# Optimization experiments

Hardware: AMD Instinct MI355X
Metric: run time of the kernel (lower is better)

## Reference

```python
import jax, jax.numpy as jnp
import numpy as np

B, NQ = 4, 4096
HF, WF = 96, 96          # single-level feature map -> Nv = 9216
NV = HF * WF
E = 768                  # dim * num_frames = 192 * 4
NH, NP, NL = 8, 4, 1
HD = E // NH             # 96
EPS = 1e-6


def _layer_norm(x, w, b):
    m = jnp.mean(x, axis=-1, keepdims=True)
    v = jnp.var(x, axis=-1, keepdims=True)
    return (x - m) * jax.lax.rsqrt(v + EPS) * w + b


def _msda_core(value, shapes, loc, aw):
    # value: (B, Nv, H, D); loc: (B, Nq, H, L, P, 2) normalized in [0,1];
    # aw: (B, Nq, H, L, P). Bilinear sampling matching F.grid_sample
    # (align_corners=False, padding_mode='zeros'): pixel = loc * size - 0.5.
    Bn, Nv, H, D = value.shape
    Nq, P = loc.shape[1], loc.shape[4]
    out = jnp.zeros((Bn, H, Nq, D), value.dtype)
    start = 0
    for lvl in range(shapes.shape[0]):
        Hl, Wl = int(shapes[lvl, 0]), int(shapes[lvl, 1])
        v = value[:, start:start + Hl * Wl].transpose(0, 2, 1, 3)  # (B,H,S,D)
        start += Hl * Wl
        x = loc[:, :, :, lvl, :, 0] * Wl - 0.5  # (B,Nq,H,P)
        y = loc[:, :, :, lvl, :, 1] * Hl - 0.5
        x0, y0 = jnp.floor(x), jnp.floor(y)
        sampled = jnp.zeros((Bn, H, Nq, P, D), value.dtype)
        for dx in (0, 1):
            for dy in (0, 1):
                xi, yi = x0 + dx, y0 + dy
                w = (1.0 - jnp.abs(x - xi)) * (1.0 - jnp.abs(y - yi))
                valid = (xi >= 0) & (xi <= Wl - 1) & (yi >= 0) & (yi <= Hl - 1)
                idx = (jnp.clip(yi, 0, Hl - 1) * Wl
                       + jnp.clip(xi, 0, Wl - 1)).astype(jnp.int32)
                idx = idx.transpose(0, 2, 1, 3).reshape(Bn, H, Nq * P)
                g = jnp.take_along_axis(v, idx[..., None], axis=2)
                g = g.reshape(Bn, H, Nq, P, D)
                wz = jnp.where(valid, w, 0.0).transpose(0, 2, 1, 3)[..., None]
                sampled = sampled + g * wz
        awl = aw[:, :, :, lvl].transpose(0, 2, 1, 3)[..., None]  # (B,H,Nq,P,1)
        out = out + jnp.sum(sampled * awl, axis=3)
    return out.transpose(0, 2, 1, 3).reshape(Bn, Nq, H * D)


def setup_inputs():
    key = jax.random.key(0)
    ks = jax.random.split(key, 12)
    s = 0.02
    return {
        "query": jax.random.normal(ks[0], (B, NQ, E), jnp.float32),
        "reference_points": jax.random.uniform(ks[1], (B, NQ, NL, 2), jnp.float32),
        "feat": jax.random.normal(ks[2], (B, NV, E), jnp.float32),
        "spatial_shapes": jnp.array([[HF, WF]], jnp.int32),
        "level_start_index": jnp.zeros((NL,), jnp.int32),
        "ln_q_w": jnp.ones((E,), jnp.float32),
        "ln_q_b": jnp.zeros((E,), jnp.float32),
        "ln_f_w": jnp.ones((E,), jnp.float32),
        "ln_f_b": jnp.zeros((E,), jnp.float32),
        "W_value": jax.random.normal(ks[3], (E, E), jnp.float32) * s,
        "b_value": jnp.zeros((E,), jnp.float32),
        "W_off": jax.random.normal(ks[4], (E, NH * NL * NP * 2), jnp.float32) * s,
        "b_off": jax.random.normal(ks[5], (NH * NL * NP * 2,), jnp.float32) * s,
        "W_attn": jax.random.normal(ks[6], (E, NH * NL * NP), jnp.float32) * s,
        "b_attn": jnp.zeros((NH * NL * NP,), jnp.float32),
        "W_out": jax.random.normal(ks[7], (E, E), jnp.float32) * s,
        "b_out": jnp.zeros((E,), jnp.float32),
        "gamma": jax.random.normal(ks[8], (E,), jnp.float32) * s,
    }


def reference(query, reference_points, feat, spatial_shapes, level_start_index,
              ln_q_w, ln_q_b, ln_f_w, ln_f_b, W_value, b_value, W_off, b_off,
              W_attn, b_attn, W_out, b_out, gamma):
    shapes = np.asarray(spatial_shapes)  # static level shapes
    Bn, Nq, _ = query.shape
    Nv = feat.shape[1]
    q = _layer_norm(query, ln_q_w, ln_q_b)
    f = _layer_norm(feat, ln_f_w, ln_f_b)
    value = (f @ W_value + b_value).reshape(Bn, Nv, NH, HD)
    offsets = (q @ W_off + b_off).reshape(Bn, Nq, NH, NL, NP, 2)
    aw = jax.nn.softmax((q @ W_attn + b_attn).reshape(Bn, Nq, NH, NL * NP), -1)
    aw = aw.reshape(Bn, Nq, NH, NL, NP)
    # offset_normalizer = [W_l, H_l] per level
    norm = jnp.stack([jnp.asarray(shapes[:, 1], jnp.float32),
                      jnp.asarray(shapes[:, 0], jnp.float32)], axis=-1)  # (L,2)
    loc = (reference_points[:, :, None, :, None, :]
           + offsets / norm[None, None, None, :, None, :])
    out = _msda_core(value, shapes, loc, aw)
    out = out @ W_out + b_out
    attn = q + out  # mmcv MSDeformAttn adds identity (dropout=eval no-op)
    return query + gamma * attn
```

## Files before the change

kernel.cpp:

```cpp
#include <hip/hip_runtime.h>

#define BB     4
#define NQS    4096
#define NVS    9216
#define E_DIM  768
#define NHEAD  8
#define NPTS   4
#define HDIM   96
#define HFEAT  96
#define WFEAT  96
#define MQR    16384
#define NLNB   13312
#define NTRB   1152
#define NVALB  432

typedef __attribute__((ext_vector_type(8))) short  s8v;
typedef __attribute__((ext_vector_type(4))) short  s4v;
typedef __attribute__((ext_vector_type(4))) float  f4v;

__device__ __forceinline__ unsigned short f2bf(float x) {
    unsigned int u = __builtin_bit_cast(unsigned int, x);
    unsigned int r = (u + 0x7fffu + ((u >> 16) & 1u)) >> 16;
    return (unsigned short)r;
}
__device__ __forceinline__ float bf2f(unsigned short s) {
    unsigned int u = ((unsigned int)s) << 16;
    return __builtin_bit_cast(float, u);
}
__device__ __forceinline__ float bf2f_s(short s) {
    return bf2f((unsigned short)s);
}

#define GLD16(gp, lp) \
    __builtin_amdgcn_global_load_lds( \
        (__attribute__((address_space(1))) void*)(gp), \
        (__attribute__((address_space(3))) void*)(lp), 16, 0, 0)

__global__ __launch_bounds__(256) void prep_kernel(
    const float* __restrict__ q, const float* __restrict__ f,
    const float* __restrict__ qw, const float* __restrict__ qb,
    const float* __restrict__ fw, const float* __restrict__ fb,
    unsigned short* __restrict__ qout, unsigned short* __restrict__ fout,
    float* __restrict__ stats,
    const float* __restrict__ W0, const float* __restrict__ W1,
    unsigned short* __restrict__ T0, unsigned short* __restrict__ T1,
    const float* __restrict__ W_off, const float* __restrict__ W_attn,
    const float* __restrict__ b_off, const float* __restrict__ b_attn,
    unsigned short* __restrict__ Wqc, float* __restrict__ bcat) {
    __shared__ float tile[32][33];
    const int bid = blockIdx.x;

    if (bid < NLNB) {
        const int wv = threadIdx.x >> 6, lane = threadIdx.x & 63;
        const int row = bid * 4 + wv;
        const bool isq = row < MQR;
        const float* x = isq ? (q + (size_t)row * E_DIM)
                             : (f + (size_t)(row - MQR) * E_DIM);
        const float4 v0 = ((const float4*)x)[lane];
        const float4 v1 = ((const float4*)x)[lane + 64];
        const float4 v2 = ((const float4*)x)[lane + 128];
        float s1 = v0.x + v0.y + v0.z + v0.w + v1.x + v1.y + v1.z + v1.w
                 + v2.x + v2.y + v2.z + v2.w;
        float s2 = v0.x * v0.x + v0.y * v0.y + v0.z * v0.z + v0.w * v0.w
                 + v1.x * v1.x + v1.y * v1.y + v1.z * v1.z + v1.w * v1.w
                 + v2.x * v2.x + v2.y * v2.y + v2.z * v2.z + v2.w * v2.w;
        #pragma unroll
        for (int o = 32; o > 0; o >>= 1) {
            s1 += __shfl_down(s1, o, 64);
            s2 += __shfl_down(s2, o, 64);
        }
        const float mean = __shfl(s1, 0, 64) * (1.0f / E_DIM);
        const float m2   = __shfl(s2, 0, 64) * (1.0f / E_DIM);
        const float rstd = rsqrtf(m2 - mean * mean + 1e-6f);
        if (isq && lane == 0) { stats[row * 2] = mean; stats[row * 2 + 1] = rstd; }
        const float* w = isq ? qw : fw;
        const float* b = isq ? qb : fb;
        unsigned short* o = isq ? (qout + (size_t)row * E_DIM)
                                : (fout + (size_t)(row - MQR) * E_DIM);
        const float4 vv[3] = {v0, v1, v2};
        #pragma unroll
        for (int c = 0; c < 3; c++) {
            const float4 w4 = ((const float4*)w)[lane + c * 64];
            const float4 b4 = ((const float4*)b)[lane + c * 64];
            s4v ov;
            ov[0] = (short)f2bf((vv[c].x - mean) * rstd * w4.x + b4.x);
            ov[1] = (short)f2bf((vv[c].y - mean) * rstd * w4.y + b4.y);
            ov[2] = (short)f2bf((vv[c].z - mean) * rstd * w4.z + b4.z);
            ov[3] = (short)f2bf((vv[c].w - mean) * rstd * w4.w + b4.w);
            ((s4v*)o)[lane + c * 64] = ov;
        }
    } else if (bid < NLNB + NTRB) {
        const int idx = bid - NLNB;
        const int z = idx / 576, r2 = idx - z * 576;
        const float* W = z ? W1 : W0;
        unsigned short* Wt = z ? T1 : T0;
        const int bi = (r2 / 24) * 32, bj = (r2 % 24) * 32;
        const int t = threadIdx.x;
        const int r = t >> 5, c = t & 31;
        #pragma unroll
        for (int i = 0; i < 4; i++)
            tile[r + i * 8][c] = W[(size_t)(bi + r + i * 8) * E_DIM + bj + c];
        __syncthreads();
        #pragma unroll
        for (int i = 0; i < 4; i++)
            Wt[(size_t)(bj + r + i * 8) * E_DIM + bi + c] = f2bf(tile[c][r + i * 8]);
    } else {
        const int idx = (bid - NLNB - NTRB) * 256 + threadIdx.x;
        const int rrow = idx / E_DIM, k = idx % E_DIM;
        float v = 0.f;
        if (rrow < 64) v = W_off[(size_t)k * 64 + rrow];
        else if (rrow < 96) v = W_attn[(size_t)k * 32 + (rrow - 64)];
        Wqc[idx] = f2bf(v);
        if (idx < 128) {
            float b = 0.f;
            if (idx < 64) b = b_off[idx];
            else if (idx < 96) b = b_attn[idx - 64];
            bcat[idx] = b;
        }
    }
}

__global__ __launch_bounds__(256, 3) void mfma_gemm128(
    const unsigned short* __restrict__ A, const unsigned short* __restrict__ Bt,
    const float* __restrict__ bias, float* __restrict__ C, int ldC,
    const float* __restrict__ query, const float* __restrict__ qstats,
    const float* __restrict__ lnw, const float* __restrict__ lnb,
    const float* __restrict__ gamma) {
    __shared__ unsigned short As[128 * 64];
    __shared__ unsigned short Bs[128 * 64];

    constexpr int K = E_DIM;
    const int tid = threadIdx.x;
    const int wave = tid >> 6;
    const int lane = tid & 63;
    const int quad = lane >> 4;
    const int l16 = lane & 15;

    const int nwg = gridDim.x * gridDim.y;
    const int flat = blockIdx.y * gridDim.x + blockIdx.x;
    const int cpx = nwg >> 3;
    const int swz = (flat & 7) * cpx + (flat >> 3);
    const int bx = swz % gridDim.x;
    const int by = swz / gridDim.x;
    const int bm = by * 128;
    const int bn = bx * 128;
    const int wrow = wave >> 1, wcol = wave & 1;

    const unsigned short* arow[4];
    const unsigned short* brow[4];
    unsigned short* aldst[4];
    unsigned short* bldst[4];
    #pragma unroll
    for (int i = 0; i < 4; i++) {
        const int chunk = wave * 4 + i;
        const int s = chunk >> 1, r = (chunk & 1) * 64 + lane;
        arow[i] = A + (size_t)(bm + r) * K + s * 8;
        brow[i] = Bt + (size_t)(bn + r) * K + s * 8;
        aldst[i] = As + chunk * 512;
        bldst[i] = Bs + chunk * 512;
    }

    f4v acc[4][4] = {};

    for (int k0 = 0; k0 < K; k0 += 64) {
        #pragma unroll
        for (int i = 0; i < 4; i++)
            GLD16(arow[i] + k0, aldst[i]);
        #pragma unroll
        for (int i = 0; i < 4; i++)
            GLD16(brow[i] + k0, bldst[i]);

        __syncthreads();

        #pragma unroll
        for (int c = 0; c < 2; c++) {
            s8v af[4], bf[4];
            #pragma unroll
            for (int ti = 0; ti < 4; ti++)
                af[ti] = *(const s8v*)(As + ((size_t)((c * 4 + quad) * 128 + wrow * 64 + ti * 16 + l16)) * 8);
            #pragma unroll
            for (int tj = 0; tj < 4; tj++)
                bf[tj] = *(const s8v*)(Bs + ((size_t)((c * 4 + quad) * 128 + wcol * 64 + tj * 16 + l16)) * 8);
            #pragma unroll
            for (int ti = 0; ti < 4; ti++)
                #pragma unroll
                for (int tj = 0; tj < 4; tj++)
                    acc[ti][tj] = __builtin_amdgcn_mfma_f32_16x16x32_bf16(af[ti], bf[tj], acc[ti][tj], 0, 0, 0);
        }
        __syncthreads();
    }

    #pragma unroll
    for (int ti = 0; ti < 4; ti++) {
        const int gm_base = bm + wrow * 64 + ti * 16 + quad * 4;
        #pragma unroll
        for (int tj = 0; tj < 4; tj++) {
            const int gn = bn + wcol * 64 + tj * 16 + l16;
            const float bv = bias[gn];
            #pragma unroll
            for (int r = 0; r < 4; r++) {
                const int gm = gm_base + r;
                const float v = acc[ti][tj][r] + bv;
                const size_t idx = (size_t)gm * ldC + gn;
                const float qv = query[idx];
                const float qln = (qv - qstats[gm * 2]) * qstats[gm * 2 + 1] * lnw[gn] + lnb[gn];
                C[idx] = qv + gamma[gn] * (qln + v);
            }
        }
    }
}

template <int G>
__device__ __forceinline__ void tigroup(const unsigned short* as_, const s8v (&bfr)[2][4],
                                        f4v (&acc)[8][4], int quad, int l16, int wrow) {
    s8v af[2][2];
    #pragma unroll
    for (int c = 0; c < 2; c++)
        #pragma unroll
        for (int m = 0; m < 2; m++)
            af[c][m] = *(const s8v*)(as_ + ((size_t)((c * 4 + quad) * 256 + wrow * 128 + (G * 2 + m) * 16 + l16)) * 8);
    #pragma unroll
    for (int c = 0; c < 2; c++)
        #pragma unroll
        for (int m = 0; m < 2; m++)
            #pragma unroll
            for (int n = 0; n < 4; n++)
                acc[G * 2 + m][n] = __builtin_amdgcn_mfma_f32_16x16x32_bf16(
                    af[c][m], bfr[c][n], acc[G * 2 + m][n], 0, 0, 0);
}

__global__ __launch_bounds__(512, 2) void mfma_gemm256(
    const unsigned short* __restrict__ A, const unsigned short* __restrict__ Bt,
    const float* __restrict__ bias, unsigned short* __restrict__ C,
    const unsigned short* __restrict__ Aq, const unsigned short* __restrict__ Wqc,
    const float* __restrict__ bcat, float* __restrict__ offattn) {
    __shared__ unsigned short As[2][256 * 64];
    __shared__ unsigned short Bs[2][256 * 64];

    constexpr int K = E_DIM;
    constexpr int NT = K / 64;
    const int tid = threadIdx.x;
    const int wave = tid >> 6;
    const int lane = tid & 63;
    const int quad = lane >> 4;
    const int l16 = lane & 15;

    if (blockIdx.x < NVALB) {
        const int flat = blockIdx.x;
        const int cpx = NVALB >> 3;
        const int swz = (flat & 7) * cpx + (flat >> 3);
        const int bx = swz % 3;
        const int by = swz / 3;
        const int bm = by * 256;
        const int bn = bx * 256;
        const int wrow = wave >> 2;
        const int wcol = wave & 3;

        const unsigned short* gsrc[4][2];
        int ldst[4][2];
        #pragma unroll
        for (int h = 0; h < 4; h++) {
            #pragma unroll
            for (int i = 0; i < 2; i++) {
                const int ch = wave * 2 + i;
                const int s = ch >> 1, rsub = ch & 1;
                const int rw = (h & 1) * 128 + rsub * 64 + lane;
                const unsigned short* base = (h < 2) ? (A + (size_t)(bm + rw) * K)
                                                     : (Bt + (size_t)(bn + rw) * K);
                gsrc[h][i] = base + s * 8;
                ldst[h][i] = (s * 256 + rw) * 8;
            }
        }

        #define STAGE256(h, kt, buf) do { \
            unsigned short* lb_ = ((h) < 2 ? &As[(buf)][0] : &Bs[(buf)][0]); \
            GLD16(gsrc[h][0] + (size_t)(kt) * 64, lb_ + ldst[h][0]); \
            GLD16(gsrc[h][1] + (size_t)(kt) * 64, lb_ + ldst[h][1]); \
        } while (0)

        f4v acc[8][4] = {};

        #pragma unroll
        for (int h = 0; h < 4; h++) STAGE256(h, 0, 0);

        int cur = 0;
        for (int t = 0; t < NT; ++t) {
            const unsigned short* as_ = &As[cur][0];
            const unsigned short* bs_ = &Bs[cur][0];
            const int nb = cur ^ 1;
            const bool pf = (t + 1 < NT);

            if (pf) {
                STAGE256(0, t + 1, nb);
                asm volatile("s_waitcnt vmcnt(2)" ::: "memory");
            } else {
                asm volatile("s_waitcnt vmcnt(0)" ::: "memory");
            }
            __builtin_amdgcn_s_barrier();
            __builtin_amdgcn_sched_barrier(0);

            s8v bfr[2][4];
            #pragma unroll
            for (int c = 0; c < 2; c++)
                #pragma unroll
                for (int n = 0; n < 4; n++)
                    bfr[c][n] = *(const s8v*)(bs_ + ((size_t)((c * 4 + quad) * 256 + wcol * 64 + n * 16 + l16)) * 8);

            __builtin_amdgcn_s_setprio(1);
            tigroup<0>(as_, bfr, acc, quad, l16, wrow);
            __builtin_amdgcn_s_setprio(0);

            if (pf) STAGE256(1, t + 1, nb);
            __builtin_amdgcn_s_setprio(1);
            tigroup<1>(as_, bfr, acc, quad, l16, wrow);
            __builtin_amdgcn_s_setprio(0);

            if (pf) STAGE256(2, t + 1, nb);
            __builtin_amdgcn_s_setprio(1);
            tigroup<2>(as_, bfr, acc, quad, l16, wrow);
            __builtin_amdgcn_s_setprio(0);

            if (pf) STAGE256(3, t + 1, nb);
            s8v af3[2][2];
            #pragma unroll
            for (int c = 0; c < 2; c++)
                #pragma unroll
                for (int m = 0; m < 2; m++)
                    af3[c][m] = *(const s8v*)(as_ + ((size_t)((c * 4 + quad) * 256 + wrow * 128 + (6 + m) * 16 + l16)) * 8);
            asm volatile("s_waitcnt lgkmcnt(0)" ::: "memory");
            __builtin_amdgcn_sched_barrier(0);
            __builtin_amdgcn_s_barrier();
            __builtin_amdgcn_sched_barrier(0);
            __builtin_amdgcn_s_setprio(1);
            #pragma unroll
            for (int c = 0; c < 2; c++)
                #pragma unroll
                for (int m = 0; m < 2; m++)
                    #pragma unroll
                    for (int n = 0; n < 4; n++)
                        acc[6 + m][n] = __builtin_amdgcn_mfma_f32_16x16x32_bf16(
                            af3[c][m], bfr[c][n], acc[6 + m][n], 0, 0, 0);
            __builtin_amdgcn_s_setprio(0);

            cur ^= 1;
        }
        #undef STAGE256

        #pragma unroll
        for (int ti = 0; ti < 8; ti++) {
            const int gm_base = bm + wrow * 128 + ti * 16 + quad * 4;
            #pragma unroll
            for (int tj = 0; tj < 4; tj++) {
                const int gn = bn + wcol * 64 + tj * 16 + l16;
                const float bv = bias[gn];
                const int hh = gn / HDIM, dd = gn - hh * HDIM;
                #pragma unroll
                for (int r = 0; r < 4; r++) {
                    const int gm = gm_base + r;
                    const float v = acc[ti][tj][r] + bv;
                    const int b = gm / NVS, s = gm - b * NVS;
                    const size_t vidx = (((size_t)b * NHEAD + hh) * NVS + s) * HDIM + dd;
                    C[vidx] = f2bf(v);
                }
            }
        }
    } else {
        const int bm = (blockIdx.x - NVALB) * 128;
        const int wrow = wave >> 2;
        const int wcol = wave & 3;
        unsigned short* As0 = &As[0][0];
        unsigned short* Bs0 = &Bs[0][0];

        const unsigned short* arow[2];
        const unsigned short* brow[2];
        int loff[2];
        #pragma unroll
        for (int i = 0; i < 2; i++) {
            const int ch = wave * 2 + i;
            const int s = ch >> 1, r = (ch & 1) * 64 + lane;
            arow[i] = Aq + (size_t)(bm + r) * K + s * 8;
            brow[i] = Wqc + (size_t)r * K + s * 8;
            loff[i] = (s * 128 + r) * 8;
        }

        f4v accq[4][2] = {};

        for (int k0 = 0; k0 < K; k0 += 64) {
            #pragma unroll
            for (int i = 0; i < 2; i++) GLD16(arow[i] + k0, As0 + loff[i]);
            #pragma unroll
            for (int i = 0; i < 2; i++) GLD16(brow[i] + k0, Bs0 + loff[i]);

            __syncthreads();

            #pragma unroll
            for (int c = 0; c < 2; c++) {
                s8v af[4], bf[2];
                #pragma unroll
                for (int m = 0; m < 4; m++)
                    af[m] = *(const s8v*)(As0 + ((size_t)((c * 4 + quad) * 128 + wrow * 64 + m * 16 + l16)) * 8);
                #pragma unroll
                for (int n = 0; n < 2; n++)
                    bf[n] = *(const s8v*)(Bs0 + ((size_t)((c * 4 + quad) * 128 + wcol * 32 + n * 16 + l16)) * 8);
                #pragma unroll
                for (int m = 0; m < 4; m++)
                    #pragma unroll
                    for (int n = 0; n < 2; n++)
                        accq[m][n] = __builtin_amdgcn_mfma_f32_16x16x32_bf16(af[m], bf[n], accq[m][n], 0, 0, 0);
            }
            __syncthreads();
        }

        #pragma unroll
        for (int m = 0; m < 4; m++) {
            const int gm_base = bm + wrow * 64 + m * 16 + quad * 4;
            #pragma unroll
            for (int n = 0; n < 2; n++) {
                const int gn = wcol * 32 + n * 16 + l16;
                const float bv = bcat[gn];
                #pragma unroll
                for (int r = 0; r < 4; r++)
                    offattn[(size_t)(gm_base + r) * 128 + gn] = accq[m][n][r] + bv;
            }
        }
    }
}

__global__ __launch_bounds__(384) void msda_kernel(
    const unsigned short* __restrict__ value,
    const float* __restrict__ oa,
    const float* __restrict__ refp,
    unsigned short* __restrict__ out) {
    const int h = blockIdx.x;
    const int row0 = blockIdx.y * 32;
    const int t = threadIdx.x;

    __shared__ float x_s[128], y_s[128], aw_s[128];
    if (t < 128) {
        const int r = t >> 2, p = t & 3;
        const int row = row0 + r;
        const float* oar = oa + (size_t)row * 128;
        float a = oar[64 + h * 4 + p];
        float mx = fmaxf(a, __shfl_xor(a, 1, 64));
        mx = fmaxf(mx, __shfl_xor(mx, 2, 64));
        float e = __expf(a - mx);
        float sden = e + __shfl_xor(e, 1, 64);
        sden += __shfl_xor(sden, 2, 64);
        aw_s[t] = e / sden;
        const float rx = refp[(size_t)row * 2 + 0] * WFEAT - 0.5f;
        const float ry = refp[(size_t)row * 2 + 1] * HFEAT - 0.5f;
        x_s[t] = rx + oar[h * 8 + p * 2 + 0];
        y_s[t] = ry + oar[h * 8 + p * 2 + 1];
    }
    __syncthreads();

    const int r = t / 12;
    const int j = t - r * 12;
    const int row = row0 + r;
    const int b = row >> 12;
    const unsigned short* vb = value + ((size_t)(b * NHEAD + h) * NVS) * HDIM + j * 8;

    float acc[8] = {};
    #pragma unroll
    for (int p = 0; p < 4; p++) {
        const float x = x_s[r * 4 + p];
        const float y = y_s[r * 4 + p];
        const float aw = aw_s[r * 4 + p];
        const float x0f = floorf(x), y0f = floorf(y);
        const float fx = x - x0f, fy = y - y0f;
        const int ix0 = (int)x0f, iy0 = (int)y0f;
        const int ix1 = ix0 + 1, iy1 = iy0 + 1;
        const float wx0 = (ix0 >= 0 && ix0 < WFEAT) ? (1.f - fx) : 0.f;
        const float wx1 = (ix1 >= 0 && ix1 < WFEAT) ? fx : 0.f;
        const float wy0 = (iy0 >= 0 && iy0 < HFEAT) ? (1.f - fy) : 0.f;
        const float wy1 = (iy1 >= 0 && iy1 < HFEAT) ? fy : 0.f;
        const int cx0 = min(max(ix0, 0), WFEAT - 1);
        const int cx1 = min(max(ix1, 0), WFEAT - 1);
        const int cy0 = min(max(iy0, 0), HFEAT - 1);
        const int cy1 = min(max(iy1, 0), HFEAT - 1);
        const float w00 = aw * wy0 * wx0, w01 = aw * wy0 * wx1;
        const float w10 = aw * wy1 * wx0, w11 = aw * wy1 * wx1;
        const s8v v00 = *(const s8v*)(vb + (size_t)(cy0 * WFEAT + cx0) * HDIM);
        const s8v v01 = *(const s8v*)(vb + (size_t)(cy0 * WFEAT + cx1) * HDIM);
        const s8v v10 = *(const s8v*)(vb + (size_t)(cy1 * WFEAT + cx0) * HDIM);
        const s8v v11 = *(const s8v*)(vb + (size_t)(cy1 * WFEAT + cx1) * HDIM);
        #pragma unroll
        for (int k = 0; k < 8; k++) {
            acc[k] += w00 * bf2f_s(v00[k]) + w01 * bf2f_s(v01[k])
                    + w10 * bf2f_s(v10[k]) + w11 * bf2f_s(v11[k]);
        }
    }

    s8v o;
    #pragma unroll
    for (int k = 0; k < 8; k++) o[k] = (short)f2bf(acc[k]);
    *(s8v*)(out + (size_t)row * E_DIM + h * HDIM + j * 8) = o;
}

extern "C" void kernel_launch(void* const* d_in, const int* in_sizes, int n_in,
                              void* d_out, int out_size, void* d_ws, size_t ws_size,
                              hipStream_t stream) {
    (void)in_sizes; (void)n_in; (void)out_size; (void)ws_size;

    const float* query  = (const float*)d_in[0];
    const float* refp   = (const float*)d_in[1];
    const float* feat   = (const float*)d_in[2];
    const float* ln_q_w = (const float*)d_in[5];
    const float* ln_q_b = (const float*)d_in[6];
    const float* ln_f_w = (const float*)d_in[7];
    const float* ln_f_b = (const float*)d_in[8];
    const float* W_val  = (const float*)d_in[9];
    const float* b_val  = (const float*)d_in[10];
    const float* W_off  = (const float*)d_in[11];
    const float* b_off  = (const float*)d_in[12];
    const float* W_attn = (const float*)d_in[13];
    const float* b_attn = (const float*)d_in[14];
    const float* W_out  = (const float*)d_in[15];
    const float* b_out  = (const float*)d_in[16];
    const float* gamma  = (const float*)d_in[17];
    float* out = (float*)d_out;

    const int MQ = BB * NQS;
    const int MV = BB * NVS;

    char* ws = (char*)d_ws;
    float*          q_stats = (float*)(ws + 0);
    unsigned short* qbf     = (unsigned short*)(ws + 131072);
    unsigned short* fbf     = (unsigned short*)(ws + 25296896);
    unsigned short* val_bf  = (unsigned short*)(ws + 81920000);
    unsigned short* msda_bf = (unsigned short*)(ws + 138543104);
    float*          offattn = (float*)(ws + 163708928);
    unsigned short* Wv_t    = (unsigned short*)(ws + 172097536);
    unsigned short* Wo_t    = (unsigned short*)(ws + 173277184);
    unsigned short* Wqc_t   = (unsigned short*)(ws + 174456832);
    float*          bcat    = (float*)(ws + 174653440);

    prep_kernel<<<NLNB + NTRB + 384, 256, 0, stream>>>(
        query, feat, ln_q_w, ln_q_b, ln_f_w, ln_f_b, qbf, fbf, q_stats,
        W_val, W_out, Wv_t, Wo_t, W_off, W_attn, b_off, b_attn, Wqc_t, bcat);

    mfma_gemm256<<<NVALB + 128, 512, 0, stream>>>(
        fbf, Wv_t, b_val, val_bf, qbf, Wqc_t, bcat, offattn);

    msda_kernel<<<dim3(NHEAD, MQ / 32), 384, 0, stream>>>(val_bf, offattn, refp, msda_bf);

    mfma_gemm128<<<dim3(E_DIM / 128, MQ / 128), 256, 0, stream>>>(
        msda_bf, Wo_t, b_out, out, E_DIM, query, q_stats, ln_q_w, ln_q_b, gamma);
}
```

Before: 442.9 us.

## Fuse deformable sampling with output projection GEMM via shared-memory tile

```diff
diff --git a/kernel.cpp b/kernel.cpp
--- a/kernel.cpp
+++ b/kernel.cpp
@@ -13,6 +13,7 @@
 #define NLNB   13312
 #define NTRB   1152
 #define NVALB  432
+#define OROWS  64
 
 typedef __attribute__((ext_vector_type(8))) short  s8v;
 typedef __attribute__((ext_vector_type(4))) short  s4v;
@@ -120,96 +121,6 @@
     }
 }
 
-__global__ __launch_bounds__(256, 3) void mfma_gemm128(
-    const unsigned short* __restrict__ A, const unsigned short* __restrict__ Bt,
-    const float* __restrict__ bias, float* __restrict__ C, int ldC,
-    const float* __restrict__ query, const float* __restrict__ qstats,
-    const float* __restrict__ lnw, const float* __restrict__ lnb,
-    const float* __restrict__ gamma) {
-    __shared__ unsigned short As[128 * 64];
-    __shared__ unsigned short Bs[128 * 64];
-
-    constexpr int K = E_DIM;
-    const int tid = threadIdx.x;
-    const int wave = tid >> 6;
-    const int lane = tid & 63;
-    const int quad = lane >> 4;
-    const int l16 = lane & 15;
-
-    const int nwg = gridDim.x * gridDim.y;
-    const int flat = blockIdx.y * gridDim.x + blockIdx.x;
-    const int cpx = nwg >> 3;
-    const int swz = (flat & 7) * cpx + (flat >> 3);
-    const int bx = swz % gridDim.x;
-    const int by = swz / gridDim.x;
-    const int bm = by * 128;
-    const int bn = bx * 128;
-    const int wrow = wave >> 1, wcol = wave & 1;
-
-    const unsigned short* arow[4];
-    const unsigned short* brow[4];
-    unsigned short* aldst[4];
-    unsigned short* bldst[4];
-    #pragma unroll
-    for (int i = 0; i < 4; i++) {
-        const int chunk = wave * 4 + i;
-        const int s = chunk >> 1, r = (chunk & 1) * 64 + lane;
-        arow[i] = A + (size_t)(bm + r) * K + s * 8;
-        brow[i] = Bt + (size_t)(bn + r) * K + s * 8;
-        aldst[i] = As + chunk * 512;
-        bldst[i] = Bs + chunk * 512;
-    }
-
-    f4v acc[4][4] = {};
-
-    for (int k0 = 0; k0 < K; k0 += 64) {
-        #pragma unroll
-        for (int i = 0; i < 4; i++)
-            GLD16(arow[i] + k0, aldst[i]);
-        #pragma unroll
-        for (int i = 0; i < 4; i++)
-            GLD16(brow[i] + k0, bldst[i]);
-
-        __syncthreads();
-
-        #pragma unroll
-        for (int c = 0; c < 2; c++) {
-            s8v af[4], bf[4];
-            #pragma unroll
-            for (int ti = 0; ti < 4; ti++)
-                af[ti] = *(const s8v*)(As + ((size_t)((c * 4 + quad) * 128 + wrow * 64 + ti * 16 + l16)) * 8);
-            #pragma unroll
-            for (int tj = 0; tj < 4; tj++)
-                bf[tj] = *(const s8v*)(Bs + ((size_t)((c * 4 + quad) * 128 + wcol * 64 + tj * 16 + l16)) * 8);
-            #pragma unroll
-            for (int ti = 0; ti < 4; ti++)
-                #pragma unroll
-                for (int tj = 0; tj < 4; tj++)
-                    acc[ti][tj] = __builtin_amdgcn_mfma_f32_16x16x32_bf16(af[ti], bf[tj], acc[ti][tj], 0, 0, 0);
-        }
-        __syncthreads();
-    }
-
-    #pragma unroll
-    for (int ti = 0; ti < 4; ti++) {
-        const int gm_base = bm + wrow * 64 + ti * 16 + quad * 4;
-        #pragma unroll
-        for (int tj = 0; tj < 4; tj++) {
-            const int gn = bn + wcol * 64 + tj * 16 + l16;
-            const float bv = bias[gn];
-            #pragma unroll
-            for (int r = 0; r < 4; r++) {
-                const int gm = gm_base + r;
-                const float v = acc[ti][tj][r] + bv;
-                const size_t idx = (size_t)gm * ldC + gn;
-                const float qv = query[idx];
-                const float qln = (qv - qstats[gm * 2]) * qstats[gm * 2 + 1] * lnw[gn] + lnb[gn];
-                C[idx] = qv + gamma[gn] * (qln + v);
-            }
-        }
-    }
-}
-
 template <int G>
 __device__ __forceinline__ void tigroup(const unsigned short* as_, const s8v (&bfr)[2][4],
                                         f4v (&acc)[8][4], int quad, int l16, int wrow) {
@@ -426,75 +337,126 @@
     }
 }
 
-__global__ __launch_bounds__(384) void msda_kernel(
+__global__ __launch_bounds__(512, 2) void msda_oproj_kernel(
     const unsigned short* __restrict__ value,
     const float* __restrict__ oa,
     const float* __restrict__ refp,
-    unsigned short* __restrict__ out) {
-    const int h = blockIdx.x;
-    const int row0 = blockIdx.y * 32;
+    const unsigned short* __restrict__ Wo,
+    const float* __restrict__ bias,
+    const float* __restrict__ query, const float* __restrict__ qstats,
+    const float* __restrict__ lnw, const float* __restrict__ lnb,
+    const float* __restrict__ gamma, float* __restrict__ out) {
+    __shared__ unsigned short Ams[OROWS * E_DIM];
+
+    const int row0 = blockIdx.x * OROWS;
     const int t = threadIdx.x;
-
-    __shared__ float x_s[128], y_s[128], aw_s[128];
-    if (t < 128) {
-        const int r = t >> 2, p = t & 3;
+    const int b = row0 >> 12;
+
+    #pragma unroll
+    for (int it = 0; it < 12; ++it) {
+        const int tt = it * 512 + t;
+        const int r = tt / 96;
+        const int rem = tt - r * 96;
+        const int h = rem / 12;
+        const int j = rem - h * 12;
         const int row = row0 + r;
         const float* oar = oa + (size_t)row * 128;
-        float a = oar[64 + h * 4 + p];
-        float mx = fmaxf(a, __shfl_xor(a, 1, 64));
-        mx = fmaxf(mx, __shfl_xor(mx, 2, 64));
-        float e = __expf(a - mx);
-        float sden = e + __shfl_xor(e, 1, 64);
-        sden += __shfl_xor(sden, 2, 64);
-        aw_s[t] = e / sden;
+        float a0 = oar[64 + h * 4 + 0], a1 = oar[64 + h * 4 + 1];
+        float a2 = oar[64 + h * 4 + 2], a3 = oar[64 + h * 4 + 3];
+        float mx = fmaxf(fmaxf(a0, a1), fmaxf(a2, a3));
+        float e0 = __expf(a0 - mx), e1 = __expf(a1 - mx);
+        float e2 = __expf(a2 - mx), e3 = __expf(a3 - mx);
+        float inv = 1.0f / (e0 + e1 + e2 + e3);
+        const float aww[4] = {e0 * inv, e1 * inv, e2 * inv, e3 * inv};
         const float rx = refp[(size_t)row * 2 + 0] * WFEAT - 0.5f;
         const float ry = refp[(size_t)row * 2 + 1] * HFEAT - 0.5f;
-        x_s[t] = rx + oar[h * 8 + p * 2 + 0];
-        y_s[t] = ry + oar[h * 8 + p * 2 + 1];
+        const unsigned short* vb = value + ((size_t)(b * NHEAD + h) * NVS) * HDIM + j * 8;
+
+        float acc[8] = {};
+        #pragma unroll
+        for (int p = 0; p < 4; p++) {
+            const float x = rx + oar[h * 8 + p * 2 + 0];
+            const float y = ry + oar[h * 8 + p * 2 + 1];
+            const float aw = aww[p];
+            const float x0f = floorf(x), y0f = floorf(y);
+            const float fx = x - x0f, fy = y - y0f;
+            const int ix0 = (int)x0f, iy0 = (int)y0f;
+            const int ix1 = ix0 + 1, iy1 = iy0 + 1;
+            const float wx0 = (ix0 >= 0 && ix0 < WFEAT) ? (1.f - fx) : 0.f;
+            const float wx1 = (ix1 >= 0 && ix1 < WFEAT) ? fx : 0.f;
+            const float wy0 = (iy0 >= 0 && iy0 < HFEAT) ? (1.f - fy) : 0.f;
+            const float wy1 = (iy1 >= 0 && iy1 < HFEAT) ? fy : 0.f;
+            const int cx0 = min(max(ix0, 0), WFEAT - 1);
+            const int cx1 = min(max(ix1, 0), WFEAT - 1);
+            const int cy0 = min(max(iy0, 0), HFEAT - 1);
+            const int cy1 = min(max(iy1, 0), HFEAT - 1);
+            const float w00 = aw * wy0 * wx0, w01 = aw * wy0 * wx1;
+            const float w10 = aw * wy1 * wx0, w11 = aw * wy1 * wx1;
+            const s8v v00 = *(const s8v*)(vb + (size_t)(cy0 * WFEAT + cx0) * HDIM);
+            const s8v v01 = *(const s8v*)(vb + (size_t)(cy0 * WFEAT + cx1) * HDIM);
+            const s8v v10 = *(const s8v*)(vb + (size_t)(cy1 * WFEAT + cx0) * HDIM);
+            const s8v v11 = *(const s8v*)(vb + (size_t)(cy1 * WFEAT + cx1) * HDIM);
+            #pragma unroll
+            for (int k = 0; k < 8; k++) {
+                acc[k] += w00 * bf2f_s(v00[k]) + w01 * bf2f_s(v01[k])
+                        + w10 * bf2f_s(v10[k]) + w11 * bf2f_s(v11[k]);
+            }
+        }
+        s8v o;
+        #pragma unroll
+        for (int k = 0; k < 8; k++) o[k] = (short)f2bf(acc[k]);
+        const int col16 = (h * 12 + j) ^ (r & 7);
+        *(s8v*)(&Ams[((size_t)r * 96 + col16) * 8]) = o;
     }
     __syncthreads();
 
-    const int r = t / 12;
-    const int j = t - r * 12;
-    const int row = row0 + r;
-    const int b = row >> 12;
-    const unsigned short* vb = value + ((size_t)(b * NHEAD + h) * NVS) * HDIM + j * 8;
-
-    float acc[8] = {};
+    const int wave = t >> 6;
+    const int lane = t & 63;
+    const int quad = lane >> 4;
+    const int l16 = lane & 15;
+
+    const unsigned short* bcol[6];
     #pragma unroll
-    for (int p = 0; p < 4; p++) {
-        const float x = x_s[r * 4 + p];
-        const float y = y_s[r * 4 + p];
-        const float aw = aw_s[r * 4 + p];
-        const float x0f = floorf(x), y0f = floorf(y);
-        const float fx = x - x0f, fy = y - y0f;
-        const int ix0 = (int)x0f, iy0 = (int)y0f;
-        const int ix1 = ix0 + 1, iy1 = iy0 + 1;
-        const float wx0 = (ix0 >= 0 && ix0 < WFEAT) ? (1.f - fx) : 0.f;
-        const float wx1 = (ix1 >= 0 && ix1 < WFEAT) ? fx : 0.f;
-        const float wy0 = (iy0 >= 0 && iy0 < HFEAT) ? (1.f - fy) : 0.f;
-        const float wy1 = (iy1 >= 0 && iy1 < HFEAT) ? fy : 0.f;
-        const int cx0 = min(max(ix0, 0), WFEAT - 1);
-        const int cx1 = min(max(ix1, 0), WFEAT - 1);
-        const int cy0 = min(max(iy0, 0), HFEAT - 1);
-        const int cy1 = min(max(iy1, 0), HFEAT - 1);
-        const float w00 = aw * wy0 * wx0, w01 = aw * wy0 * wx1;
-        const float w10 = aw * wy1 * wx0, w11 = aw * wy1 * wx1;
-        const s8v v00 = *(const s8v*)(vb + (size_t)(cy0 * WFEAT + cx0) * HDIM);
-        const s8v v01 = *(const s8v*)(vb + (size_t)(cy0 * WFEAT + cx1) * HDIM);
-        const s8v v10 = *(const s8v*)(vb + (size_t)(cy1 * WFEAT + cx0) * HDIM);
-        const s8v v11 = *(const s8v*)(vb + (size_t)(cy1 * WFEAT + cx1) * HDIM);
-        #pragma unroll
-        for (int k = 0; k < 8; k++) {
-            acc[k] += w00 * bf2f_s(v00[k]) + w01 * bf2f_s(v01[k])
-                    + w10 * bf2f_s(v10[k]) + w11 * bf2f_s(v11[k]);
-        }
+    for (int n = 0; n < 6; n++)
+        bcol[n] = Wo + (size_t)(wave * 96 + n * 16 + l16) * E_DIM + quad * 8;
+
+    f4v acc[4][6] = {};
+
+    for (int k0 = 0; k0 < E_DIM; k0 += 32) {
+        const int kc = (k0 >> 3) + quad;
+        s8v af[4], bf[6];
+        #pragma unroll
+        for (int m = 0; m < 4; m++) {
+            const int r = m * 16 + l16;
+            af[m] = *(const s8v*)(&Ams[((size_t)r * 96 + (kc ^ (r & 7))) * 8]);
+        }
+        #pragma unroll
+        for (int n = 0; n < 6; n++)
+            bf[n] = *(const s8v*)(bcol[n] + k0);
+        #pragma unroll
+        for (int m = 0; m < 4; m++)
+            #pragma unroll
+            for (int n = 0; n < 6; n++)
+                acc[m][n] = __builtin_amdgcn_mfma_f32_16x16x32_bf16(af[m], bf[n], acc[m][n], 0, 0, 0);
     }
 
-    s8v o;
     #pragma unroll
-    for (int k = 0; k < 8; k++) o[k] = (short)f2bf(acc[k]);
-    *(s8v*)(out + (size_t)row * E_DIM + h * HDIM + j * 8) = o;
+    for (int m = 0; m < 4; m++) {
+        const int gm_base = row0 + m * 16 + quad * 4;
+        #pragma unroll
+        for (int n = 0; n < 6; n++) {
+            const int gn = wave * 96 + n * 16 + l16;
+            const float bv = bias[gn];
+            #pragma unroll
+            for (int r = 0; r < 4; r++) {
+                const int gm = gm_base + r;
+                const size_t idx = (size_t)gm * E_DIM + gn;
+                const float qv = query[idx];
+                const float qln = (qv - qstats[gm * 2]) * qstats[gm * 2 + 1] * lnw[gn] + lnb[gn];
+                out[idx] = qv + gamma[gn] * (qln + acc[m][n][r] + bv);
+            }
+        }
+    }
 }
 
 extern "C" void kernel_launch(void* const* d_in, const int* in_sizes, int n_in,
@@ -528,7 +490,6 @@
     unsigned short* qbf     = (unsigned short*)(ws + 131072);
     unsigned short* fbf     = (unsigned short*)(ws + 25296896);
     unsigned short* val_bf  = (unsigned short*)(ws + 81920000);
-    unsigned short* msda_bf = (unsigned short*)(ws + 138543104);
     float*          offattn = (float*)(ws + 163708928);
     unsigned short* Wv_t    = (unsigned short*)(ws + 172097536);
     unsigned short* Wo_t    = (unsigned short*)(ws + 173277184);
@@ -542,8 +503,7 @@
     mfma_gemm256<<<NVALB + 128, 512, 0, stream>>>(
         fbf, Wv_t, b_val, val_bf, qbf, Wqc_t, bcat, offattn);
 
-    msda_kernel<<<dim3(NHEAD, MQ / 32), 384, 0, stream>>>(val_bf, offattn, refp, msda_bf);
-
-    mfma_gemm128<<<dim3(E_DIM / 128, MQ / 128), 256, 0, stream>>>(
-        msda_bf, Wo_t, b_out, out, E_DIM, query, q_stats, ln_q_w, ln_q_b, gamma);
-}
+    msda_oproj_kernel<<<MQ / OROWS, 512, 0, stream>>>(
+        val_bf, offattn, refp, Wo_t, b_out, query, q_stats, ln_q_w, ln_q_b,
+        gamma, out);
+}
```

Measured after the change: 419.0 us. -5.4%, faster.
